# Performance work log

Hardware: AMD Instinct MI355X
Metric: run time of the kernel (lower is better)

## Reference

```python
import jax, jax.numpy as jnp
import numpy as np

LN_EPS = 1e-5

def setup_inputs() -> dict:
    key = jax.random.key(0)
    k1, k2, k3, k4 = jax.random.split(key, 4)
    B, N, D, E = 2, 50000, 128, 800000
    H = jax.random.normal(k1, (B, N, D), dtype=jnp.float32)
    src = jax.random.randint(k2, (E,), 0, N, dtype=jnp.int64)
    dst = jax.random.randint(k3, (E,), 0, N, dtype=jnp.int64)
    W = jax.random.normal(k4, (D, D), dtype=jnp.float32) * (1.0 / np.sqrt(D))
    gamma = jnp.ones((D,), dtype=jnp.float32)
    beta = jnp.zeros((D,), dtype=jnp.float32)
    return {"H": H, "src": src, "dst": dst, "W": W, "gamma": gamma, "beta": beta}

def reference(H, src, dst, W, gamma, beta):
    # m = Linear(H) (no bias): [B,N,D]
    m = jnp.einsum('bnd,de->bne', H, W)
    # gather messages at src, scatter-add into dst along node dim
    agg = jnp.zeros_like(m).at[:, dst, :].add(m[:, src, :])
    x = H + jax.nn.gelu(agg, approximate=False)
    # LayerNorm over last dim
    mu = jnp.mean(x, axis=-1, keepdims=True)
    var = jnp.var(x, axis=-1, keepdims=True)
    return (x - mu) * jax.lax.rsqrt(var + LN_EPS) * gamma + beta
```

## Files before the change

kernel.cpp:

```cpp
#include <hip/hip_runtime.h>
#include <math.h>

#define DIM 128
#define LN_EPS 1e-5f
#define CAP 64

typedef unsigned short bf16_t;
typedef unsigned short u16;
typedef __attribute__((ext_vector_type(8))) short bf16x8;
typedef __attribute__((ext_vector_type(4))) float f32x4;

__device__ __forceinline__ bf16_t f2bf(float f) {
    unsigned u = __builtin_bit_cast(unsigned, f);
    u += 0x7FFFu + ((u >> 16) & 1u);
    return (bf16_t)(u >> 16);
}
__device__ __forceinline__ float bf2f(bf16_t h) {
    unsigned u = ((unsigned)h) << 16;
    return __builtin_bit_cast(float, u);
}

__global__ __launch_bounds__(256) void prep_kernel(
    const float* __restrict__ W, bf16_t* __restrict__ WT,
    int* __restrict__ cursor, int N)
{
    const int tid = blockIdx.x * 256 + threadIdx.x;
    if (tid < N) cursor[tid] = 0;
    if (tid < (DIM * DIM / 4)) {
        const float4 w = ((const float4*)W)[tid];
        const int k  = tid >> 5;
        const int n0 = (tid & 31) * 4;
        WT[(n0 + 0) * DIM + k] = f2bf(w.x);
        WT[(n0 + 1) * DIM + k] = f2bf(w.y);
        WT[(n0 + 2) * DIM + k] = f2bf(w.z);
        WT[(n0 + 3) * DIM + k] = f2bf(w.w);
    }
}

__global__ __launch_bounds__(256) void gemm_fill_kernel(
    const float* __restrict__ Hmat, const bf16_t* __restrict__ WT,
    bf16_t* __restrict__ Mout,
    const int* __restrict__ src, const int* __restrict__ dst,
    int* __restrict__ cursor, u16* __restrict__ eidxT,
    int nrows, int N, int E, int FB)
{
    if ((int)blockIdx.x < FB) {
        int e = blockIdx.x * 256 + threadIdx.x;
        if (e < E) {
            int d = dst[e];
            int pos = atomicAdd(&cursor[d], 1);
            if (pos < CAP) eidxT[(size_t)pos * N + d] = (u16)src[e];
        }
        return;
    }

    const int tid = threadIdx.x;
    const int gblock = blockIdx.x - FB;

    const int wave = tid >> 6;
    const int lane = tid & 63;
    const int quad = lane >> 4;
    const int l15  = lane & 15;

    const int arow = gblock * 64 + wave * 16 + l15;
    const float* Arow = Hmat + (size_t)((arow < nrows) ? arow : 0) * DIM;
    const bf16_t* Bbase = WT + (size_t)l15 * DIM;

    f32x4 acc[8];
    #pragma unroll
    for (int t = 0; t < 8; ++t) acc[t] = (f32x4){0.f, 0.f, 0.f, 0.f};

    #pragma unroll
    for (int ks = 0; ks < 4; ++ks) {
        const int k0 = ks * 32 + quad * 8;
        float4 a0 = *(const float4*)&Arow[k0];
        float4 a1 = *(const float4*)&Arow[k0 + 4];
        bf16x8 af;
        af[0] = (short)f2bf(a0.x); af[1] = (short)f2bf(a0.y);
        af[2] = (short)f2bf(a0.z); af[3] = (short)f2bf(a0.w);
        af[4] = (short)f2bf(a1.x); af[5] = (short)f2bf(a1.y);
        af[6] = (short)f2bf(a1.z); af[7] = (short)f2bf(a1.w);

        #pragma unroll
        for (int t = 0; t < 8; ++t) {
            bf16x8 bf = *(const bf16x8*)&Bbase[t * 16 * DIM + k0];
            acc[t] = __builtin_amdgcn_mfma_f32_16x16x32_bf16(af, bf, acc[t], 0, 0, 0);
        }
    }

    const int outrowbase = gblock * 64 + wave * 16 + quad * 4;
    #pragma unroll
    for (int r = 0; r < 4; ++r) {
        int rr = outrowbase + r;
        if (rr < nrows) {
            int b = (rr >= N) ? 1 : 0;
            int n = rr - (b ? N : 0);
            bf16_t* orow = Mout + ((size_t)n * 2 + b) * DIM + l15;
            #pragma unroll
            for (int t = 0; t < 8; ++t)
                orow[t * 16] = f2bf(acc[t][r]);
        }
    }
}

__global__ __launch_bounds__(256) void gather_kernel(
    const bf16_t* __restrict__ M, const float* __restrict__ Hmat,
    const int* __restrict__ cursor, const u16* __restrict__ eidxT,
    const float* __restrict__ gamma, const float* __restrict__ beta,
    float* __restrict__ out, int N)
{
    const int wave = threadIdx.x >> 6;
    const int lane = threadIdx.x & 63;
    const int node = blockIdx.x * 4 + wave;
    if (node >= N) return;

    const int b  = lane >> 5;
    const int c4 = lane & 31;

    int cnt = cursor[node];
    if (cnt > CAP) cnt = CAP;

    int myidx = (lane < cnt) ? (int)eidxT[(size_t)lane * N + node] : 0;

    const ushort4* M4 = (const ushort4*)M;

    float acc0 = 0.f, acc1 = 0.f, acc2 = 0.f, acc3 = 0.f;
    int j = 0;
    for (; j + 8 <= cnt; j += 8) {
        ushort4 v[8];
        #pragma unroll
        for (int q = 0; q < 8; ++q) {
            int s = __shfl(myidx, j + q, 64);
            v[q] = M4[(size_t)s * 64 + lane];
        }
        #pragma unroll
        for (int q = 0; q < 8; ++q) {
            acc0 += bf2f(v[q].x); acc1 += bf2f(v[q].y);
            acc2 += bf2f(v[q].z); acc3 += bf2f(v[q].w);
        }
    }
    for (; j < cnt; ++j) {
        int s = __shfl(myidx, j, 64);
        ushort4 v0 = M4[(size_t)s * 64 + lane];
        acc0 += bf2f(v0.x); acc1 += bf2f(v0.y);
        acc2 += bf2f(v0.z); acc3 += bf2f(v0.w);
    }

    const size_t elembase = ((size_t)b * N + node) * DIM + c4 * 4;
    float4 h = *(const float4*)&Hmat[elembase];
    const float inv_sqrt2 = 0.70710678118654752f;
    float x0 = h.x + 0.5f * acc0 * (1.f + erff(acc0 * inv_sqrt2));
    float x1 = h.y + 0.5f * acc1 * (1.f + erff(acc1 * inv_sqrt2));
    float x2 = h.z + 0.5f * acc2 * (1.f + erff(acc2 * inv_sqrt2));
    float x3 = h.w + 0.5f * acc3 * (1.f + erff(acc3 * inv_sqrt2));

    float s  = x0 + x1 + x2 + x3;
    float ss = x0 * x0 + x1 * x1 + x2 * x2 + x3 * x3;
    #pragma unroll
    for (int o = 16; o > 0; o >>= 1) {
        s  += __shfl_xor(s,  o, 64);
        ss += __shfl_xor(ss, o, 64);
    }
    const float mean = s * (1.f / DIM);
    const float var  = ss * (1.f / DIM) - mean * mean;
    const float inv  = rsqrtf(var + LN_EPS);

    float4 gm = *(const float4*)&gamma[c4 * 4];
    float4 bt = *(const float4*)&beta[c4 * 4];
    float4 o;
    o.x = (x0 - mean) * inv * gm.x + bt.x;
    o.y = (x1 - mean) * inv * gm.y + bt.y;
    o.z = (x2 - mean) * inv * gm.z + bt.z;
    o.w = (x3 - mean) * inv * gm.w + bt.w;
    *(float4*)&out[elembase] = o;
}

extern "C" void kernel_launch(void* const* d_in, const int* in_sizes, int n_in,
                              void* d_out, int out_size, void* d_ws, size_t ws_size,
                              hipStream_t stream)
{
    const float* H     = (const float*)d_in[0];
    const int*   src   = (const int*)  d_in[1];
    const int*   dst   = (const int*)  d_in[2];
    const float* W     = (const float*)d_in[3];
    const float* gamma = (const float*)d_in[4];
    const float* beta  = (const float*)d_in[5];
    float* out = (float*)d_out;

    const int E     = in_sizes[1];
    const int total = in_sizes[0];
    const int nrows = total / DIM;
    const int N     = nrows / 2;

    char* ws = (char*)d_ws;
    bf16_t* Mbuf = (bf16_t*)ws;   ws += (size_t)total * sizeof(bf16_t);
    int* cursor  = (int*)ws;      ws += (size_t)N * sizeof(int);
    u16* eidxT   = (u16*)ws;      ws += (size_t)CAP * N * sizeof(u16);
    bf16_t* WT   = (bf16_t*)ws;   ws += (size_t)DIM * DIM * sizeof(bf16_t);

    const int FB = (E + 255) / 256;
    const int GB = (nrows + 63) / 64;

    int prep_elems = (N > DIM * DIM / 4) ? N : DIM * DIM / 4;
    prep_kernel<<<(prep_elems + 255) / 256, 256, 0, stream>>>(W, WT, cursor, N);

    gemm_fill_kernel<<<FB + GB, 256, 0, stream>>>(H, WT, Mbuf, src, dst,
                                                  cursor, eidxT, nrows, N, E, FB);

    gather_kernel<<<(N + 3) / 4, 256, 0, stream>>>(Mbuf, H, cursor, eidxT,
                                                   gamma, beta, out, N);
}
```

Baseline: 233.0 us.

## Split fill from GEMM, keep W fragments in registers, swap MFMA operands

Separates the edge-bucketing fill and the GEMM into two kernel launches. The GEMM now loads all W fragments into registers once per wave and reuses them across TPW row tiles. It also swaps the MFMA operand order so each lane holds 4 contiguous output columns, which lets it write them as ushort4 instead of scalar bf16 stores. The cost is an extra launch, the lost overlap between the atomic fill and the GEMM, and higher register pressure from 32 bf16x8 fragments.

```diff
diff --git a/kernel.cpp b/kernel.cpp
--- a/kernel.cpp
+++ b/kernel.cpp
@@ -4,6 +4,7 @@
 #define DIM 128
 #define LN_EPS 1e-5f
 #define CAP 64
+#define TPW 2
 
 typedef unsigned short bf16_t;
 typedef unsigned short u16;
@@ -37,68 +38,75 @@
     }
 }
 
-__global__ __launch_bounds__(256) void gemm_fill_kernel(
+__global__ __launch_bounds__(256) void fill_kernel(
+    const int* __restrict__ src, const int* __restrict__ dst,
+    int* __restrict__ cursor, u16* __restrict__ eidxT, int N, int E)
+{
+    int e = blockIdx.x * 256 + threadIdx.x;
+    if (e < E) {
+        int d = dst[e];
+        int pos = atomicAdd(&cursor[d], 1);
+        if (pos < CAP) eidxT[(size_t)pos * N + d] = (u16)src[e];
+    }
+}
+
+__global__ __launch_bounds__(256) void gemm_kernel(
     const float* __restrict__ Hmat, const bf16_t* __restrict__ WT,
-    bf16_t* __restrict__ Mout,
-    const int* __restrict__ src, const int* __restrict__ dst,
-    int* __restrict__ cursor, u16* __restrict__ eidxT,
-    int nrows, int N, int E, int FB)
-{
-    if ((int)blockIdx.x < FB) {
-        int e = blockIdx.x * 256 + threadIdx.x;
-        if (e < E) {
-            int d = dst[e];
-            int pos = atomicAdd(&cursor[d], 1);
-            if (pos < CAP) eidxT[(size_t)pos * N + d] = (u16)src[e];
-        }
-        return;
-    }
-
-    const int tid = threadIdx.x;
-    const int gblock = blockIdx.x - FB;
-
+    bf16_t* __restrict__ Mout, int nrows, int N)
+{
+    const int tid  = threadIdx.x;
     const int wave = tid >> 6;
     const int lane = tid & 63;
     const int quad = lane >> 4;
     const int l15  = lane & 15;
 
-    const int arow = gblock * 64 + wave * 16 + l15;
-    const float* Arow = Hmat + (size_t)((arow < nrows) ? arow : 0) * DIM;
-    const bf16_t* Bbase = WT + (size_t)l15 * DIM;
-
-    f32x4 acc[8];
+    bf16x8 wf[32];
     #pragma unroll
-    for (int t = 0; t < 8; ++t) acc[t] = (f32x4){0.f, 0.f, 0.f, 0.f};
+    for (int t = 0; t < 8; ++t)
+        #pragma unroll
+        for (int ks = 0; ks < 4; ++ks)
+            wf[t * 4 + ks] = *(const bf16x8*)
+                &WT[(size_t)(t * 16 + l15) * DIM + ks * 32 + quad * 8];
+
+    const int baserow = (blockIdx.x * 4 + wave) * (TPW * 16);
 
     #pragma unroll
-    for (int ks = 0; ks < 4; ++ks) {
-        const int k0 = ks * 32 + quad * 8;
-        float4 a0 = *(const float4*)&Arow[k0];
-        float4 a1 = *(const float4*)&Arow[k0 + 4];
-        bf16x8 af;
-        af[0] = (short)f2bf(a0.x); af[1] = (short)f2bf(a0.y);
-        af[2] = (short)f2bf(a0.z); af[3] = (short)f2bf(a0.w);
-        af[4] = (short)f2bf(a1.x); af[5] = (short)f2bf(a1.y);
-        af[6] = (short)f2bf(a1.z); af[7] = (short)f2bf(a1.w);
-
-        #pragma unroll
-        for (int t = 0; t < 8; ++t) {
-            bf16x8 bf = *(const bf16x8*)&Bbase[t * 16 * DIM + k0];
-            acc[t] = __builtin_amdgcn_mfma_f32_16x16x32_bf16(af, bf, acc[t], 0, 0, 0);
-        }
-    }
-
-    const int outrowbase = gblock * 64 + wave * 16 + quad * 4;
-    #pragma unroll
-    for (int r = 0; r < 4; ++r) {
-        int rr = outrowbase + r;
-        if (rr < nrows) {
-            int b = (rr >= N) ? 1 : 0;
-            int n = rr - (b ? N : 0);
-            bf16_t* orow = Mout + ((size_t)n * 2 + b) * DIM + l15;
+    for (int rt = 0; rt < TPW; ++rt) {
+        const int arow = baserow + rt * 16 + l15;
+        const float* Arow = Hmat + (size_t)((arow < nrows) ? arow : 0) * DIM;
+
+        f32x4 acc[8];
+        #pragma unroll
+        for (int t = 0; t < 8; ++t) acc[t] = (f32x4){0.f, 0.f, 0.f, 0.f};
+
+        #pragma unroll
+        for (int ks = 0; ks < 4; ++ks) {
+            const int k0 = ks * 32 + quad * 8;
+            float4 a0 = *(const float4*)&Arow[k0];
+            float4 a1 = *(const float4*)&Arow[k0 + 4];
+            bf16x8 hf;
+            hf[0] = (short)f2bf(a0.x); hf[1] = (short)f2bf(a0.y);
+            hf[2] = (short)f2bf(a0.z); hf[3] = (short)f2bf(a0.w);
+            hf[4] = (short)f2bf(a1.x); hf[5] = (short)f2bf(a1.y);
+            hf[6] = (short)f2bf(a1.z); hf[7] = (short)f2bf(a1.w);
+
             #pragma unroll
             for (int t = 0; t < 8; ++t)
-                orow[t * 16] = f2bf(acc[t][r]);
+                acc[t] = __builtin_amdgcn_mfma_f32_16x16x32_bf16(
+                             wf[t * 4 + ks], hf, acc[t], 0, 0, 0);
+        }
+
+        if (arow < nrows) {
+            const int b = (arow >= N) ? 1 : 0;
+            const int n = arow - (b ? N : 0);
+            bf16_t* orow = Mout + ((size_t)n * 2 + b) * DIM;
+            #pragma unroll
+            for (int t = 0; t < 8; ++t) {
+                ushort4 o;
+                o.x = f2bf(acc[t][0]); o.y = f2bf(acc[t][1]);
+                o.z = f2bf(acc[t][2]); o.w = f2bf(acc[t][3]);
+                *(ushort4*)&orow[t * 16 + quad * 4] = o;
+            }
         }
     }
 }
@@ -198,14 +206,14 @@
     u16* eidxT   = (u16*)ws;      ws += (size_t)CAP * N * sizeof(u16);
     bf16_t* WT   = (bf16_t*)ws;   ws += (size_t)DIM * DIM * sizeof(bf16_t);
 
-    const int FB = (E + 255) / 256;
-    const int GB = (nrows + 63) / 64;
-
     int prep_elems = (N > DIM * DIM / 4) ? N : DIM * DIM / 4;
     prep_kernel<<<(prep_elems + 255) / 256, 256, 0, stream>>>(W, WT, cursor, N);
 
-    gemm_fill_kernel<<<FB + GB, 256, 0, stream>>>(H, WT, Mbuf, src, dst,
-                                                  cursor, eidxT, nrows, N, E, FB);
+    fill_kernel<<<(E + 255) / 256, 256, 0, stream>>>(src, dst, cursor, eidxT, N, E);
+
+    const int ROWS_PER_BLOCK = 4 * TPW * 16;
+    gemm_kernel<<<(nrows + ROWS_PER_BLOCK - 1) / ROWS_PER_BLOCK, 256, 0, stream>>>(
+        H, WT, Mbuf, nrows, N);
 
     gather_kernel<<<(N + 3) / 4, 256, 0, stream>>>(Mbuf, H, cursor, eidxT,
                                                    gamma, beta, out, N);
```

Result: no change. 232.4 us (-0.3%).
